# Kernel optimization log

Hardware: AMD Instinct MI355X
Metric: run time of the kernel (lower is better)

The kernel has to match this reference:

```python
import jax, jax.numpy as jnp
import numpy as np

EPS = 1e-5  # torch InstanceNorm2d default
C = 512

def setup_inputs() -> dict:
    key = jax.random.key(0)
    ks = jax.random.split(key, 9)
    x = jax.random.normal(ks[0], (4, C, 64, 64), dtype=jnp.float32)
    s = 0.05
    wq = jax.random.normal(ks[1], (C, C), dtype=jnp.float32) * s
    wk = jax.random.normal(ks[2], (C, C), dtype=jnp.float32) * s
    wv = jax.random.normal(ks[3], (C, C), dtype=jnp.float32) * s
    wp = jax.random.normal(ks[4], (C, C), dtype=jnp.float32) * s
    bq = jax.random.normal(ks[5], (C,), dtype=jnp.float32) * s
    bk = jax.random.normal(ks[6], (C,), dtype=jnp.float32) * s
    bv = jax.random.normal(ks[7], (C,), dtype=jnp.float32) * s
    bp = jax.random.normal(ks[8], (C,), dtype=jnp.float32) * s
    return {"x": x, "wq": wq, "bq": bq, "wk": wk, "bk": bk,
            "wv": wv, "bv": bv, "wp": wp, "bp": bp}

def _conv1x1(h, w, b):
    # 1x1 conv == per-pixel channel mixing: (b,c,h,w) x (o,c) -> (b,o,h,w)
    return jnp.einsum('bchw,oc->bohw', h, w) + b[None, :, None, None]

def reference(x, wq, bq, wk, bk, wv, bv, wp, bp):
    b, c, h, w = x.shape
    # InstanceNorm2d (affine=False): normalize each (b,c) plane over spatial dims
    mu = jnp.mean(x, axis=(2, 3), keepdims=True)
    var = jnp.mean(jnp.square(x - mu), axis=(2, 3), keepdims=True)
    hn = (x - mu) * jax.lax.rsqrt(var + EPS)
    q = _conv1x1(hn, wq, bq).reshape(b, c, h * w)
    k = _conv1x1(hn, wk, bk).reshape(b, c, h * w)
    v = _conv1x1(hn, wv, bv).reshape(b, c, h * w)
    # attn[b,i,j] = <q[:, i], k[:, j]> / sqrt(c), softmax over keys j
    attn = jnp.einsum('bci,bcj->bij', q, k) / jnp.sqrt(jnp.asarray(c, x.dtype))
    attn = jax.nn.softmax(attn, axis=2)
    # out[b,c,i] = sum_j v[b,c,j] * attn[b,i,j]
    o = jnp.einsum('bcj,bij->bci', v, attn).reshape(b, c, h, w)
    return x + _conv1x1(o, wp, bp)
```

## Files before the change

kernel.cpp:

```cpp
#include <hip/hip_runtime.h>
#include <hip/hip_bf16.h>

typedef short bf16x8 __attribute__((ext_vector_type(8)));
typedef float f32x4 __attribute__((ext_vector_type(4)));

#define CCH 512
#define NPIX 4096
#define NB 4

__device__ inline unsigned short f2bf(float f) {
  union { __hip_bfloat16 h; unsigned short u; } cv;
  cv.h = __float2bfloat16(f);
  return cv.u;
}

#define GLD16(gp, lp) __builtin_amdgcn_global_load_lds( \
    (const __attribute__((address_space(1))) unsigned int*)(gp), \
    (__attribute__((address_space(3))) unsigned int*)(lp), 16, 0, 0)

__global__ __launch_bounds__(256) void cast_weights_k(
    const float* __restrict__ w0, const float* __restrict__ w1,
    const float* __restrict__ w2, const float* __restrict__ w3,
    unsigned short* __restrict__ out) {
  int z = blockIdx.y;
  const float* src = (z == 0) ? w0 : (z == 1) ? w1 : (z == 2) ? w2 : w3;
  long i = (long)blockIdx.x * 256 + threadIdx.x;
  out[(long)z * CCH * CCH + i] = f2bf(src[i]);
}

__global__ __launch_bounds__(256) void bias_concat_k(
    const float* __restrict__ bq, const float* __restrict__ bk,
    float* __restrict__ bqk) {
  int i = blockIdx.x * 256 + threadIdx.x;
  bqk[i] = (i < CCH) ? bq[i] : bk[i - CCH];
}

__global__ __launch_bounds__(256) void zero_l_k(float* __restrict__ lsum) {
  int i = (blockIdx.x * 256 + threadIdx.x) * 4;
  *(float4*)(lsum + i) = make_float4(0.f, 0.f, 0.f, 0.f);
}

__global__ __launch_bounds__(256) void stats_k(const float* __restrict__ x,
                                               float* __restrict__ stats) {
  long plane = blockIdx.x;
  const float4* p = (const float4*)(x + plane * NPIX);
  int t = threadIdx.x;
  float s = 0.f, q = 0.f;
  for (int c = 0; c < 4; c++) {
    float4 v = p[c * 256 + t];
    s += v.x + v.y + v.z + v.w;
    q += v.x * v.x + v.y * v.y + v.z * v.z + v.w * v.w;
  }
  for (int off = 32; off; off >>= 1) { s += __shfl_xor(s, off); q += __shfl_xor(q, off); }
  __shared__ float rs[4], rq[4];
  int w = t >> 6;
  if ((t & 63) == 0) { rs[w] = s; rq[w] = q; }
  __syncthreads();
  if (t == 0) {
    s = rs[0] + rs[1] + rs[2] + rs[3];
    q = rq[0] + rq[1] + rq[2] + rq[3];
    float mu = s * (1.f / NPIX);
    float var = q * (1.f / NPIX) - mu * mu;
    stats[2 * plane] = mu;
    stats[2 * plane + 1] = rsqrtf(var + 1e-5f);
  }
}

__global__ __launch_bounds__(256) void norm_t_k(const float* __restrict__ x,
                                                const float* __restrict__ stats,
                                                unsigned short* __restrict__ hnT) {
  int b = blockIdx.z;
  int c0 = blockIdx.y * 32, i0 = blockIdx.x * 32;
  __shared__ float tile[32][33];
  int t = threadIdx.x;
  int il = t & 31, cl = t >> 5;
  for (int r = 0; r < 4; r++) {
    int c = c0 + cl + r * 8;
    long pl = (long)b * CCH + c;
    float mu = stats[2 * pl], rsg = stats[2 * pl + 1];
    tile[cl + r * 8][il] = (x[pl * NPIX + i0 + il] - mu) * rsg;
  }
  __syncthreads();
  for (int r = 0; r < 4; r++) {
    int i = i0 + cl + r * 8;
    hnT[((long)b * NPIX + i) * CCH + c0 + il] = f2bf(tile[il][cl + r * 8]);
  }
}

template <int OUTF32, int BIASM, bool RESID, bool SCALE, bool EXPSUM, bool ROWSCALE>
__global__ __launch_bounds__(256) void gemm_bt_k(
    const unsigned short* __restrict__ A, const unsigned short* __restrict__ B,
    void* __restrict__ Cv, const float* __restrict__ bias,
    const float* __restrict__ resid, float* __restrict__ lsum,
    int K, int lda, int ldb, int ldc,
    long sA, long sB, long sC, float scale) {
  int z = blockIdx.z;
  A += z * sA;
  B += z * sB;
  const int n0 = blockIdx.x * 128, m0 = blockIdx.y * 128;
  const int t = threadIdx.x;
  const int lane = t & 63, w = t >> 6;
  const int wr = w >> 1, wc = w & 1;

  __shared__ __align__(16) unsigned short LDS[2][2][128 * 64];

  f32x4 acc[4][4] = {};

  const int srow = t >> 3;
  const int scol = (((t & 7) ^ (srow & 7)) * 8);
  const unsigned short* ga = A + (long)(m0 + srow) * lda + scol;
  const unsigned short* gb = B + (long)(n0 + srow) * ldb + scol;
  const long stpa = (long)32 * lda;
  const long stpb = (long)32 * ldb;

#define STAGE(bb, kt) do {                                                   \
    const unsigned short* gak = ga + (long)(kt) * 64;                        \
    const unsigned short* gbk = gb + (long)(kt) * 64;                        \
    char* la = (char*)&LDS[bb][0][0] + t * 16;                               \
    char* lb = (char*)&LDS[bb][1][0] + t * 16;                               \
    GLD16(gak, la);                                                          \
    GLD16(gak + stpa, la + 4096);                                            \
    GLD16(gak + 2 * stpa, la + 8192);                                        \
    GLD16(gak + 3 * stpa, la + 12288);                                       \
    GLD16(gbk, lb);                                                          \
    GLD16(gbk + stpb, lb + 4096);                                            \
    GLD16(gbk + 2 * stpb, lb + 8192);                                        \
    GLD16(gbk + 3 * stpb, lb + 12288);                                       \
  } while (0)

  const int fr = lane & 15, fq = lane >> 4;
  const int chx = fr & 7;
  const int rAo = (wr * 64 + fr) * 64;
  const int rBo = (wc * 64 + fr) * 64;

  const int nkt = K >> 6;
  STAGE(0, 0);
  int cur = 0;
  for (int kt = 0; kt < nkt; kt++) {
    if (kt + 1 < nkt) {
      STAGE(cur ^ 1, kt + 1);
      asm volatile("s_waitcnt vmcnt(8)" ::: "memory");
    } else {
      asm volatile("s_waitcnt vmcnt(0)" ::: "memory");
    }
    __builtin_amdgcn_s_barrier();
    const unsigned short* rA = &LDS[cur][0][rAo];
    const unsigned short* rB = &LDS[cur][1][rBo];
    for (int kk = 0; kk < 2; kk++) {
      const int offA = ((fq + kk * 4) ^ chx) * 8;
      bf16x8 af[4], bfr[4];
      for (int i = 0; i < 4; i++) af[i] = *(const bf16x8*)(rA + i * 1024 + offA);
      for (int i = 0; i < 4; i++) bfr[i] = *(const bf16x8*)(rB + i * 1024 + offA);
      for (int i = 0; i < 4; i++)
        for (int j = 0; j < 4; j++)
          acc[i][j] = __builtin_amdgcn_mfma_f32_16x16x32_bf16(af[i], bfr[j], acc[i][j], 0, 0, 0);
    }
    __builtin_amdgcn_s_barrier();
    cur ^= 1;
  }
#undef STAGE

  if (OUTF32) {
    float* Cf = (float*)Cv;
    for (int i = 0; i < 4; i++) {
      int mg = m0 + wr * 64 + i * 16 + fq * 4;
      for (int j = 0; j < 4; j++) {
        int ng = n0 + wc * 64 + j * 16 + fr;
        for (int r = 0; r < 4; r++) {
          float v = acc[i][j][r];
          if (SCALE) v *= scale;
          int m = mg + r;
          if (BIASM == 1) v += bias[m];
          else if (BIASM == 2) v += bias[ng];
          long off = z * sC + (long)m * ldc + ng;
          if (RESID) v += resid[off];
          Cf[off] = v;
        }
      }
    }
  } else {
    float linv[4][4];
    if (ROWSCALE) {
      for (int i = 0; i < 4; i++)
        for (int r = 0; r < 4; r++)
          linv[i][r] = 1.f / lsum[z * NPIX + m0 + wr * 64 + i * 16 + fq * 4 + r];
    }
    float rsum[4][4];
    if (EXPSUM) {
      for (int i = 0; i < 4; i++)
        for (int r = 0; r < 4; r++) rsum[i][r] = 0.f;
    }
    unsigned short* Cb = (unsigned short*)Cv;
    for (int i = 0; i < 4; i++) {
      int mg = m0 + wr * 64 + i * 16 + fq * 4;
      for (int j = 0; j < 4; j++) {
        int ng = n0 + wc * 64 + j * 16 + fr;
        for (int r = 0; r < 4; r++) {
          float v = acc[i][j][r];
          if (SCALE) v *= scale;
          if (BIASM == 1) v += bias[mg + r];
          else if (BIASM == 2) v += bias[ng];
          if (EXPSUM) { v = exp2f(v); rsum[i][r] += v; }
          if (ROWSCALE) v *= linv[i][r];
          Cb[z * sC + (long)(mg + r) * ldc + ng] = f2bf(v);
        }
      }
    }
    if (EXPSUM) {
      for (int i = 0; i < 4; i++)
        for (int r = 0; r < 4; r++) {
          float s = rsum[i][r];
          s += __shfl_xor(s, 1);
          s += __shfl_xor(s, 2);
          s += __shfl_xor(s, 4);
          s += __shfl_xor(s, 8);
          if (fr == 0)
            atomicAdd(&lsum[z * NPIX + m0 + wr * 64 + i * 16 + fq * 4 + r], s);
        }
    }
  }
}

extern "C" void kernel_launch(void* const* d_in, const int* in_sizes, int n_in,
                              void* d_out, int out_size, void* d_ws, size_t ws_size,
                              hipStream_t stream) {
  const float* x  = (const float*)d_in[0];
  const float* wq = (const float*)d_in[1];
  const float* bq = (const float*)d_in[2];
  const float* wk = (const float*)d_in[3];
  const float* bk = (const float*)d_in[4];
  const float* wv = (const float*)d_in[5];
  const float* bv = (const float*)d_in[6];
  const float* wp = (const float*)d_in[7];
  const float* bp = (const float*)d_in[8];

  char* ws = (char*)d_ws;
  const long SLAB = (long)NPIX * CCH;
  const long SLAB2 = (long)NPIX * 1024;
  const long SLABP = (long)NPIX * NPIX;

  float* stats = (float*)ws;
  float* bqk = (float*)(ws + (32l << 10));
  float* lsum = (float*)(ws + (64l << 10));
  unsigned short* wbf = (unsigned short*)(ws + (192l << 10));
  unsigned short* hnT = (unsigned short*)(ws + (192l << 10) + (1l << 21));
  unsigned short* QKt = hnT + 4 * SLAB;
  unsigned short* V   = QKt + 4 * SLAB2;
  unsigned short* Ot  = V + 4 * SLAB;
  unsigned short* S4  = Ot + 4 * SLAB;

  unsigned short* wv_bf = wbf + 2 * 262144;
  unsigned short* wp_bf = wbf + 3 * 262144;

  cast_weights_k<<<dim3(1024, 4, 1), 256, 0, stream>>>(wq, wk, wv, wp, wbf);
  bias_concat_k<<<dim3(4, 1, 1), 256, 0, stream>>>(bq, bk, bqk);
  zero_l_k<<<dim3(16, 1, 1), 256, 0, stream>>>(lsum);
  stats_k<<<dim3(NB * CCH, 1, 1), 256, 0, stream>>>(x, stats);
  norm_t_k<<<dim3(128, 16, 4), 256, 0, stream>>>(x, stats, hnT);

  gemm_bt_k<0, 2, false, false, false, false><<<dim3(8, 32, 4), 256, 0, stream>>>(
      hnT, wbf, QKt, bqk, nullptr, nullptr, 512, 512, 512, 1024, SLAB, 0, SLAB2, 1.f);
  gemm_bt_k<0, 1, false, false, false, false><<<dim3(32, 4, 4), 256, 0, stream>>>(
      wv_bf, hnT, V, bv, nullptr, nullptr, 512, 512, 512, 4096, 0, SLAB, SLAB, 1.f);

  const float isc2 = 0.06375871387551278f;
  gemm_bt_k<0, 0, false, true, true, false><<<dim3(32, 32, 4), 256, 0, stream>>>(
      QKt, QKt + 512, S4, nullptr, nullptr, lsum, 512, 1024, 1024, 4096,
      SLAB2, SLAB2, SLABP, isc2);
  gemm_bt_k<0, 0, false, false, false, true><<<dim3(4, 32, 4), 256, 0, stream>>>(
      S4, V, Ot, nullptr, nullptr, lsum, 4096, 4096, 4096, 512, SLABP, SLAB, SLAB, 1.f);
  gemm_bt_k<1, 1, true, false, false, false><<<dim3(32, 4, 4), 256, 0, stream>>>(
      wp_bf, Ot, d_out, bp, x, nullptr, 512, 512, 512, 4096, 0, SLAB, SLAB, 1.f);
}
```

Measured before the change: 326.2 us.

## Enlarge GEMM tiles to 256x256/128x256 with 512-thread blocks

New measurement: 340.2 us. 4.3% more time.

```diff
diff --git a/kernel.cpp b/kernel.cpp
--- a/kernel.cpp
+++ b/kernel.cpp
@@ -87,51 +87,53 @@
   }
 }
 
-template <int OUTF32, int BIASM, bool RESID, bool SCALE, bool EXPSUM, bool ROWSCALE>
-__global__ __launch_bounds__(256) void gemm_bt_k(
+template <int BM, int OUTF32, int BIASM, bool RESID, bool SCALE, bool EXPSUM, bool ROWSCALE>
+__global__ __launch_bounds__(512) void gemm_bt_k(
     const unsigned short* __restrict__ A, const unsigned short* __restrict__ B,
     void* __restrict__ Cv, const float* __restrict__ bias,
     const float* __restrict__ resid, float* __restrict__ lsum,
     int K, int lda, int ldb, int ldc,
     long sA, long sB, long sC, float scale) {
+  constexpr int BN = 256;
+  constexpr int MR = BM / 32;
+  constexpr int NR = 4;
+  constexpr int ALD = BM / 64;
+  constexpr int BLD = BN / 64;
   int z = blockIdx.z;
   A += z * sA;
   B += z * sB;
-  const int n0 = blockIdx.x * 128, m0 = blockIdx.y * 128;
+  const int n0 = blockIdx.x * BN, m0 = blockIdx.y * BM;
   const int t = threadIdx.x;
   const int lane = t & 63, w = t >> 6;
-  const int wr = w >> 1, wc = w & 1;
-
-  __shared__ __align__(16) unsigned short LDS[2][2][128 * 64];
-
-  f32x4 acc[4][4] = {};
+  const int wr = w >> 2, wc = w & 3;
+
+  __shared__ __align__(16) unsigned short LA[2][BM * 64];
+  __shared__ __align__(16) unsigned short LB[2][BN * 64];
+
+  f32x4 acc[MR][NR] = {};
 
   const int srow = t >> 3;
   const int scol = (((t & 7) ^ (srow & 7)) * 8);
   const unsigned short* ga = A + (long)(m0 + srow) * lda + scol;
   const unsigned short* gb = B + (long)(n0 + srow) * ldb + scol;
-  const long stpa = (long)32 * lda;
-  const long stpb = (long)32 * ldb;
+  const long stpa = (long)64 * lda;
+  const long stpb = (long)64 * ldb;
 
 #define STAGE(bb, kt) do {                                                   \
     const unsigned short* gak = ga + (long)(kt) * 64;                        \
     const unsigned short* gbk = gb + (long)(kt) * 64;                        \
-    char* la = (char*)&LDS[bb][0][0] + t * 16;                               \
-    char* lb = (char*)&LDS[bb][1][0] + t * 16;                               \
-    GLD16(gak, la);                                                          \
-    GLD16(gak + stpa, la + 4096);                                            \
-    GLD16(gak + 2 * stpa, la + 8192);                                        \
-    GLD16(gak + 3 * stpa, la + 12288);                                       \
-    GLD16(gbk, lb);                                                          \
-    GLD16(gbk + stpb, lb + 4096);                                            \
-    GLD16(gbk + 2 * stpb, lb + 8192);                                        \
-    GLD16(gbk + 3 * stpb, lb + 12288);                                       \
+    char* la = (char*)&LA[bb][0] + t * 16;                                   \
+    char* lb = (char*)&LB[bb][0] + t * 16;                                   \
+    _Pragma("unroll")                                                        \
+    for (int p = 0; p < ALD; p++) GLD16(gak + p * stpa, la + p * 8192);      \
+    _Pragma("unroll")                                                        \
+    for (int p = 0; p < BLD; p++) GLD16(gbk + p * stpb, lb + p * 8192);      \
   } while (0)
 
   const int fr = lane & 15, fq = lane >> 4;
   const int chx = fr & 7;
-  const int rAo = (wr * 64 + fr) * 64;
-  const int rBo = (wc * 64 + fr) * 64;
+  const int rAbase = (wr * (BM / 2) + fr) * 64;
+  const int rBbase = (wc * 64 + fr) * 64;
 
   const int nkt = K >> 6;
   STAGE(0, 0);
@@ -139,22 +141,34 @@
   for (int kt = 0; kt < nkt; kt++) {
     if (kt + 1 < nkt) {
       STAGE(cur ^ 1, kt + 1);
-      asm volatile("s_waitcnt vmcnt(8)" ::: "memory");
+      if (BM == 256)
+        asm volatile("s_waitcnt vmcnt(8)" ::: "memory");
+      else
+        asm volatile("s_waitcnt vmcnt(6)" ::: "memory");
     } else {
       asm volatile("s_waitcnt vmcnt(0)" ::: "memory");
     }
     __builtin_amdgcn_s_barrier();
-    const unsigned short* rA = &LDS[cur][0][rAo];
-    const unsigned short* rB = &LDS[cur][1][rBo];
-    for (int kk = 0; kk < 2; kk++) {
-      const int offA = ((fq + kk * 4) ^ chx) * 8;
-      bf16x8 af[4], bfr[4];
-      for (int i = 0; i < 4; i++) af[i] = *(const bf16x8*)(rA + i * 1024 + offA);
-      for (int i = 0; i < 4; i++) bfr[i] = *(const bf16x8*)(rB + i * 1024 + offA);
-      for (int i = 0; i < 4; i++)
-        for (int j = 0; j < 4; j++)
-          acc[i][j] = __builtin_amdgcn_mfma_f32_16x16x32_bf16(af[i], bfr[j], acc[i][j], 0, 0, 0);
-    }
+    const unsigned short* la_ = &LA[cur][0];
+    const unsigned short* lb_ = &LB[cur][0];
+    __builtin_amdgcn_s_setprio(1);
+    bf16x8 bfr[NR][2];
+#pragma unroll
+    for (int n = 0; n < NR; n++) {
+      bfr[n][0] = *(const bf16x8*)(lb_ + rBbase + n * 1024 + (fq ^ chx) * 8);
+      bfr[n][1] = *(const bf16x8*)(lb_ + rBbase + n * 1024 + ((fq + 4) ^ chx) * 8);
+    }
+#pragma unroll
+    for (int m = 0; m < MR; m++) {
+      bf16x8 a0 = *(const bf16x8*)(la_ + rAbase + m * 1024 + (fq ^ chx) * 8);
+      bf16x8 a1 = *(const bf16x8*)(la_ + rAbase + m * 1024 + ((fq + 4) ^ chx) * 8);
+#pragma unroll
+      for (int n = 0; n < NR; n++) {
+        acc[m][n] = __builtin_amdgcn_mfma_f32_16x16x32_bf16(a0, bfr[n][0], acc[m][n], 0, 0, 0);
+        acc[m][n] = __builtin_amdgcn_mfma_f32_16x16x32_bf16(a1, bfr[n][1], acc[m][n], 0, 0, 0);
+      }
+    }
+    __builtin_amdgcn_s_setprio(0);
     __builtin_amdgcn_s_barrier();
     cur ^= 1;
   }
@@ -162,9 +176,9 @@
 
   if (OUTF32) {
     float* Cf = (float*)Cv;
-    for (int i = 0; i < 4; i++) {
-      int mg = m0 + wr * 64 + i * 16 + fq * 4;
-      for (int j = 0; j < 4; j++) {
+    for (int i = 0; i < MR; i++) {
+      int mg = m0 + wr * (BM / 2) + i * 16 + fq * 4;
+      for (int j = 0; j < NR; j++) {
         int ng = n0 + wc * 64 + j * 16 + fr;
         for (int r = 0; r < 4; r++) {
           float v = acc[i][j][r];
@@ -179,21 +193,21 @@
       }
     }
   } else {
-    float linv[4][4];
+    float linv[MR][4];
     if (ROWSCALE) {
-      for (int i = 0; i < 4; i++)
+      for (int i = 0; i < MR; i++)
         for (int r = 0; r < 4; r++)
-          linv[i][r] = 1.f / lsum[z * NPIX + m0 + wr * 64 + i * 16 + fq * 4 + r];
-    }
-    float rsum[4][4];
+          linv[i][r] = 1.f / lsum[z * NPIX + m0 + wr * (BM / 2) + i * 16 + fq * 4 + r];
+    }
+    float rsum[MR][4];
     if (EXPSUM) {
-      for (int i = 0; i < 4; i++)
+      for (int i = 0; i < MR; i++)
         for (int r = 0; r < 4; r++) rsum[i][r] = 0.f;
     }
     unsigned short* Cb = (unsigned short*)Cv;
-    for (int i = 0; i < 4; i++) {
-      int mg = m0 + wr * 64 + i * 16 + fq * 4;
-      for (int j = 0; j < 4; j++) {
+    for (int i = 0; i < MR; i++) {
+      int mg = m0 + wr * (BM / 2) + i * 16 + fq * 4;
+      for (int j = 0; j < NR; j++) {
         int ng = n0 + wc * 64 + j * 16 + fr;
         for (int r = 0; r < 4; r++) {
           float v = acc[i][j][r];
@@ -207,7 +221,7 @@
       }
     }
     if (EXPSUM) {
-      for (int i = 0; i < 4; i++)
+      for (int i = 0; i < MR; i++)
         for (int r = 0; r < 4; r++) {
           float s = rsum[i][r];
           s += __shfl_xor(s, 1);
@@ -215,7 +229,7 @@
           s += __shfl_xor(s, 4);
           s += __shfl_xor(s, 8);
           if (fr == 0)
-            atomicAdd(&lsum[z * NPIX + m0 + wr * 64 + i * 16 + fq * 4 + r], s);
+            atomicAdd(&lsum[z * NPIX + m0 + wr * (BM / 2) + i * 16 + fq * 4 + r], s);
         }
     }
   }
@@ -258,17 +272,17 @@
   stats_k<<<dim3(NB * CCH, 1, 1), 256, 0, stream>>>(x, stats);
   norm_t_k<<<dim3(128, 16, 4), 256, 0, stream>>>(x, stats, hnT);
 
-  gemm_bt_k<0, 2, false, false, false, false><<<dim3(8, 32, 4), 256, 0, stream>>>(
+  gemm_bt_k<256, 0, 2, false, false, false, false><<<dim3(4, 16, 4), 512, 0, stream>>>(
       hnT, wbf, QKt, bqk, nullptr, nullptr, 512, 512, 512, 1024, SLAB, 0, SLAB2, 1.f);
-  gemm_bt_k<0, 1, false, false, false, false><<<dim3(32, 4, 4), 256, 0, stream>>>(
+  gemm_bt_k<128, 0, 1, false, false, false, false><<<dim3(16, 4, 4), 512, 0, stream>>>(
       wv_bf, hnT, V, bv, nullptr, nullptr, 512, 512, 512, 4096, 0, SLAB, SLAB, 1.f);
 
   const float isc2 = 0.06375871387551278f;
-  gemm_bt_k<0, 0, false, true, true, false><<<dim3(32, 32, 4), 256, 0, stream>>>(
+  gemm_bt_k<256, 0, 0, false, true, true, false><<<dim3(16, 16, 4), 512, 0, stream>>>(
       QKt, QKt + 512, S4, nullptr, nullptr, lsum, 512, 1024, 1024, 4096,
       SLAB2, SLAB2, SLABP, isc2);
-  gemm_bt_k<0, 0, false, false, false, true><<<dim3(4, 32, 4), 256, 0, stream>>>(
+  gemm_bt_k<256, 0, 0, false, false, false, true><<<dim3(2, 16, 4), 512, 0, stream>>>(
       S4, V, Ot, nullptr, nullptr, lsum, 4096, 4096, 4096, 512, SLABP, SLAB, SLAB, 1.f);
-  gemm_bt_k<1, 1, true, false, false, false><<<dim3(32, 4, 4), 256, 0, stream>>>(
+  gemm_bt_k<128, 1, 1, true, false, false, false><<<dim3(16, 4, 4), 512, 0, stream>>>(
       wp_bf, Ot, d_out, bp, x, nullptr, 512, 512, 512, 4096, 0, SLAB, SLAB, 1.f);
 }
```
